# Performance work log

Measured on AMD Instinct MI355X. Metric: run time of the kernel, lower is better.

The kernel has to match this reference:

```python
import math
import jax, jax.numpy as jnp
import numpy as np

N, B, C, H, K = 1024, 8, 512, 8, 5  # seq len, batch, d_model, heads, near_kth
NEG = -1.0e9


def setup_inputs() -> dict:
    key = jax.random.key(0)
    ks = jax.random.split(key, 10)
    s = 0.02
    return {
        "query": jax.random.normal(ks[0], (N, B, C), jnp.float32),
        "key_t": jax.random.normal(ks[1], (N, B, C), jnp.float32),
        "value": jax.random.normal(ks[2], (N, B, C), jnp.float32),
        "src_position": jax.random.normal(ks[3], (N, B, 3), jnp.float32),
        "tgt_position": jax.random.normal(ks[4], (N, B, 3), jnp.float32),
        # nn.MultiheadAttention params (in_proj split into q/k/v, plus out_proj)
        "Wq": jax.random.normal(ks[5], (C, C), jnp.float32) * s,
        "Wk": jax.random.normal(ks[6], (C, C), jnp.float32) * s,
        "Wv": jax.random.normal(ks[7], (C, C), jnp.float32) * s,
        "bq": jnp.zeros((C,), jnp.float32),
        "bk": jnp.zeros((C,), jnp.float32),
        "bv": jnp.zeros((C,), jnp.float32),
        "Wo": jax.random.normal(ks[8], (C, C), jnp.float32) * s,
        "bo": jnp.zeros((C,), jnp.float32),
    }


def reference(query, key_t, value, src_position, tgt_position,
              Wq, Wk, Wv, bq, bk, bv, Wo, bo):
    # --- 'nearby' positional mask ---------------------------------------
    # dist[b, tgt, src] = ||src_position[src,b] - tgt_position[tgt,b]||^2
    diff = src_position[None, :, :, :] - tgt_position[:, None, :, :]  # (Nt,Ns,B,3)
    dist = jnp.sum(diff * diff, axis=-1).transpose(2, 0, 1)           # (B,Nt,Ns)
    # torch: topk(dist, k=5, dim=1, largest=False) -> 5 nearest TARGETS per source
    _, idx = jax.lax.top_k(-dist.transpose(0, 2, 1), K)               # (B,Ns,K) tgt idx
    mask = jnp.full((B, N, N), NEG, jnp.float32)
    b_i = jnp.arange(B)[:, None, None]
    s_i = jnp.arange(N)[None, :, None]
    mask = mask.at[b_i, idx, s_i].set(0.0)                            # (B,Nt,Ns)

    # --- multihead attention (eval mode, dropout=0) ----------------------
    hd = C // H
    scale = 1.0 / math.sqrt(hd)
    q = ((query @ Wq.T + bq) * scale).reshape(N, B, H, hd)
    k = (key_t @ Wk.T + bk).reshape(N, B, H, hd)
    v = (value @ Wv.T + bv).reshape(N, B, H, hd)
    scores = jnp.einsum('tbhd,sbhd->bhts', q, k) + mask[:, None]      # (B,H,Nt,Ns)
    attn = jax.nn.softmax(scores, axis=-1)
    ctx = jnp.einsum('bhts,sbhd->tbhd', attn, v).reshape(N, B, C)
    out = ctx @ Wo.T + bo                                             # (N,B,C)
    attn_avg = attn.mean(axis=1)                                      # (B,Nt,Ns)
    return out, attn_avg
```

## Files before the change

kernel.cpp:

```cpp
#include <hip/hip_runtime.h>
#include <cstdint>
#include <cstddef>

#define NSEQ 1024
#define BATCH 8
#define CMODEL 512
#define NHEAD 8
#define HDIM 64
#define CAP 64
#define FLTMAX 3.402823466e+38f

typedef short bf16x8 __attribute__((ext_vector_type(8)));
typedef float f32x4 __attribute__((ext_vector_type(4)));
typedef unsigned short ushort8v __attribute__((ext_vector_type(8)));
typedef unsigned short ushort2v __attribute__((ext_vector_type(2)));
typedef unsigned long long u64;

__device__ inline unsigned short f2bf(float f) {
    unsigned int u = __builtin_bit_cast(unsigned int, f);
    u += 0x7fffu + ((u >> 16) & 1u);
    return (unsigned short)(u >> 16);
}
__device__ inline float bf2f(unsigned short u) {
    return __builtin_bit_cast(float, (unsigned int)u << 16);
}

#define GLDS16(gsrc, ldst) \
    __builtin_amdgcn_global_load_lds((const __attribute__((address_space(1))) void*)(gsrc), \
                                     (__attribute__((address_space(3))) void*)(ldst), 16, 0, 0)

__global__ __launch_bounds__(256) void prepA(const float* __restrict__ w0,
                                             const float* __restrict__ w1,
                                             const float* __restrict__ w2,
                                             const float* __restrict__ w3,
                                             const float* __restrict__ value,
                                             const float* __restrict__ tgtp,
                                             const float* __restrict__ srcp,
                                             unsigned short* __restrict__ o0,
                                             unsigned short* __restrict__ o1,
                                             unsigned short* __restrict__ o2,
                                             unsigned short* __restrict__ o3,
                                             unsigned int* __restrict__ zp,
                                             float* __restrict__ vm_raw,
                                             float* __restrict__ tgt_soa,
                                             float* __restrict__ src_soa) {
    const int bid = blockIdx.x;
    const int tid = threadIdx.x;
    if (bid < 512) {
        const int idx = bid * 256 + tid;
        const int seg = idx >> 15;
        const int c   = idx & 32767;
        const float* src = seg == 0 ? w0 : seg == 1 ? w1 : seg == 2 ? w2 : w3;
        unsigned short* dst = seg == 0 ? o0 : seg == 1 ? o1 : seg == 2 ? o2 : o3;
        const float4 v0 = *(const float4*)(src + (size_t)c * 8);
        const float4 v1 = *(const float4*)(src + (size_t)c * 8 + 4);
        ushort8v u;
        u[0] = f2bf(v0.x); u[1] = f2bf(v0.y); u[2] = f2bf(v0.z); u[3] = f2bf(v0.w);
        u[4] = f2bf(v1.x); u[5] = f2bf(v1.y); u[6] = f2bf(v1.z); u[7] = f2bf(v1.w);
        *(ushort8v*)(dst + (size_t)c * 8) = u;
        return;
    }
    if (bid < 544) {
        zp[(bid - 512) * 256 + tid] = 0u;
        return;
    }
    if (bid < 608) {
        const int cb = bid - 544;
        const int b = cb >> 3, cg = cb & 7;
        const int ts = tid >> 6, c = cg * 64 + (tid & 63);
        float s = 0.f;
        for (int i = 0; i < 256; ++i) {
            const int t = ts * 256 + i;
            s += value[((size_t)t * BATCH + b) * CMODEL + c];
        }
        __shared__ float sh[4][64];
        sh[ts][tid & 63] = s;
        __syncthreads();
        if (ts == 0)
            vm_raw[b * CMODEL + c] = sh[0][tid & 63] + sh[1][tid & 63] +
                                     sh[2][tid & 63] + sh[3][tid & 63];
        return;
    }
    const int tb = bid - 608;
    const int which = tb >> 3, b = tb & 7;
    const float* src = which == 0 ? tgtp : srcp;
    float* dst = which == 0 ? tgt_soa : src_soa;
    for (int t = tid; t < NSEQ; t += 256) {
        const float* p = src + ((size_t)t * BATCH + b) * 3;
        dst[(b * 3 + 0) * NSEQ + t] = p[0];
        dst[(b * 3 + 1) * NSEQ + t] = p[1];
        dst[(b * 3 + 2) * NSEQ + t] = p[2];
    }
}

#define CX64(a, b) { const bool _c = (a) < (b); const u64 _mn = _c ? (a) : (b); \
                     const u64 _mx = _c ? (b) : (a); (a) = _mn; (b) = _mx; }

__global__ __launch_bounds__(256) void megaB(const float* __restrict__ a0,
                                             const float* __restrict__ a1,
                                             const float* __restrict__ a2,
                                             unsigned short* __restrict__ oa0,
                                             unsigned short* __restrict__ oa1,
                                             unsigned short* __restrict__ oa2,
                                             const float* __restrict__ src_soa,
                                             const float* __restrict__ tgt_soa,
                                             int* __restrict__ row_cnt,
                                             int* __restrict__ row_list,
                                             const unsigned short* __restrict__ Wv,
                                             const float* __restrict__ bv,
                                             const float* __restrict__ vm_raw,
                                             float* __restrict__ vm) {
    const int p = blockIdx.x;
    const int tid = threadIdx.x;

    if (p < 32) {
        const int bsel = p >> 2, quad = p & 3;
        const int w = tid >> 6, lane = tid & 63;
        const float* vr = vm_raw + bsel * CMODEL;
        const float4 va = *(const float4*)(vr + lane * 8);
        const float4 vb = *(const float4*)(vr + lane * 8 + 4);
        float vp[8] = {va.x, va.y, va.z, va.w, vb.x, vb.y, vb.z, vb.w};
        for (int i = 0; i < 32; ++i) {
            const int c = quad * 128 + w * 32 + i;
            const ushort8v wv = *(const ushort8v*)(Wv + (size_t)c * CMODEL + lane * 8);
            float s = 0.f;
            #pragma unroll
            for (int j = 0; j < 8; ++j) s += vp[j] * bf2f(wv[j]);
            #pragma unroll
            for (int off = 1; off < 64; off <<= 1) s += __shfl_xor(s, off);
            if (lane == 0) vm[bsel * CMODEL + c] = s * (1.f / (float)NSEQ) + bv[c];
        }
        return;
    }

    if (p >= 2080) {
        const unsigned int idx = (unsigned int)(p - 2080) * 256u + tid;
        const unsigned int seg = idx >> 19;
        const unsigned int c   = idx & 524287u;
        const float* src = seg == 0 ? a0 : seg == 1 ? a1 : a2;
        unsigned short* dst = seg == 0 ? oa0 : seg == 1 ? oa1 : oa2;
        const float4 v0 = *(const float4*)(src + (size_t)c * 8);
        const float4 v1 = *(const float4*)(src + (size_t)c * 8 + 4);
        ushort8v u;
        u[0] = f2bf(v0.x); u[1] = f2bf(v0.y); u[2] = f2bf(v0.z); u[3] = f2bf(v0.w);
        u[4] = f2bf(v1.x); u[5] = f2bf(v1.y); u[6] = f2bf(v1.z); u[7] = f2bf(v1.w);
        *(ushort8v*)(dst + (size_t)c * 8) = u;
        return;
    }

    const int w = tid >> 6, lane = tid & 63;
    const int wg = (p - 32) * 4 + w;
    const int s = wg & 1023, b = wg >> 10;

    const float* tx = tgt_soa + (b * 3 + 0) * NSEQ;
    const float* ty = tgt_soa + (b * 3 + 1) * NSEQ;
    const float* tz = tgt_soa + (b * 3 + 2) * NSEQ;
    const float sx = src_soa[(b * 3 + 0) * NSEQ + s];
    const float sy = src_soa[(b * 3 + 1) * NSEQ + s];
    const float sz = src_soa[(b * 3 + 2) * NSEQ + s];

    u64 v0 = ~0ull, v1 = ~0ull, v2 = ~0ull, v3 = ~0ull, v4 = ~0ull;

    #pragma unroll
    for (int i = 0; i < 16; ++i) {
        const int t = i * 64 + lane;
        const float dx = tx[t] - sx;
        const float dy = ty[t] - sy;
        const float dz = tz[t] - sz;
        const float d = dx * dx + dy * dy + dz * dz;
        u64 x = ((u64)__builtin_bit_cast(unsigned int, d) << 32) | (unsigned int)t;
        if (x < v4) {
            CX64(v0, x);
            CX64(v1, x);
            CX64(v2, x);
            CX64(v3, x);
            CX64(v4, x);
        }
    }

    #pragma unroll
    for (int off = 1; off < 64; off <<= 1) {
        const u64 p0 = __shfl_xor(v4, off);
        const u64 p1 = __shfl_xor(v3, off);
        const u64 p2 = __shfl_xor(v2, off);
        const u64 p3 = __shfl_xor(v1, off);
        const u64 p4 = __shfl_xor(v0, off);
        v0 = v0 < p0 ? v0 : p0;
        v1 = v1 < p1 ? v1 : p1;
        v2 = v2 < p2 ? v2 : p2;
        v3 = v3 < p3 ? v3 : p3;
        v4 = v4 < p4 ? v4 : p4;
        CX64(v0, v1); CX64(v3, v4); CX64(v2, v4); CX64(v2, v3); CX64(v1, v4);
        CX64(v0, v3); CX64(v0, v2); CX64(v1, v3); CX64(v1, v2);
    }

    if (lane == 0) {
        const u64 win[5] = {v0, v1, v2, v3, v4};
        #pragma unroll
        for (int k = 0; k < 5; ++k) {
            const int tt = (int)(unsigned int)win[k];
            const int pos = atomicAdd(&row_cnt[b * NSEQ + tt], 1);
            if (pos < CAP) row_list[((size_t)b * NSEQ + tt) * CAP + pos] = s;
        }
    }
}

__global__ __launch_bounds__(256, 3) void gemm_proj(const unsigned short* __restrict__ Aq,
                                                    const unsigned short* __restrict__ Ak,
                                                    const unsigned short* __restrict__ Av,
                                                    const unsigned short* __restrict__ Wq,
                                                    const unsigned short* __restrict__ Wk,
                                                    const unsigned short* __restrict__ Wv,
                                                    const float* __restrict__ bq,
                                                    const float* __restrict__ bk,
                                                    const float* __restrict__ bv,
                                                    unsigned short* __restrict__ oq,
                                                    unsigned short* __restrict__ ok,
                                                    unsigned short* __restrict__ ov) {
    __shared__ __align__(16) unsigned short smem[3 * 8192];
    const int p = blockIdx.x;
    const int logical = (p & 7) * 96 + (p >> 3);
    const int z = logical >> 8;
    const int r = logical & 255;
    const int m0 = (r >> 2) * 128, n0 = (r & 3) * 128;
    const unsigned short* Abf = z == 0 ? Aq : z == 1 ? Ak : Av;
    const unsigned short* Wbf = z == 0 ? Wq : z == 1 ? Wk : Wv;
    const float* bias = z == 0 ? bq : z == 1 ? bk : bv;
    unsigned short* outp = z == 0 ? oq : z == 1 ? ok : ov;
    const float scale = z == 0 ? 0.125f : 1.0f;

    const int tid = threadIdx.x;
    const int l = tid & 63, w = tid >> 6;
    const int wr = (w >> 1) * 64, wc = (w & 1) * 64;
    const int lr = l & 15, g = l >> 4;

    f32x4 acc[4][4] = {};

    const int rowX = tid >> 2;
    const int kg0  = (tid & 3) ^ ((rowX >> 1) & 3);
    const unsigned short* aS0 = Abf + (size_t)(m0 + rowX) * CMODEL + kg0 * 8;
    const unsigned short* aS1 = aS0 + (size_t)64 * CMODEL;
    const unsigned short* bS0 = Wbf + (size_t)(n0 + rowX) * CMODEL + kg0 * 8;
    const unsigned short* bS1 = bS0 + (size_t)64 * CMODEL;
    const int wb = w * 512;

    auto STAGE = [&](int k0, int buf) {
        unsigned short* bb = smem + buf * 8192;
        GLDS16(aS0 + k0, bb + wb);
        GLDS16(aS1 + k0, bb + 2048 + wb);
        GLDS16(bS0 + k0, bb + 4096 + wb);
        GLDS16(bS1 + k0, bb + 6144 + wb);
    };
    auto COMPUTE = [&](const unsigned short* base) {
        bf16x8 af[4], bg[4];
        #pragma unroll
        for (int i = 0; i < 4; ++i) {
            const int ra = wr + i * 16 + lr;
            af[i] = *(const bf16x8*)(base + ra * 32 + ((g ^ ((ra >> 1) & 3)) << 3));
        }
        #pragma unroll
        for (int j = 0; j < 4; ++j) {
            const int rb = wc + j * 16 + lr;
            bg[j] = *(const bf16x8*)(base + 4096 + rb * 32 + ((g ^ ((rb >> 1) & 3)) << 3));
        }
        #pragma unroll
        for (int i = 0; i < 4; ++i)
            #pragma unroll
            for (int j = 0; j < 4; ++j)
                acc[i][j] = __builtin_amdgcn_mfma_f32_16x16x32_bf16(af[i], bg[j], acc[i][j], 0, 0, 0);
    };

    STAGE(0, 0);
    STAGE(32, 1);

    int cur = 0;
    for (int t = 0; t < 15; ++t) {
        asm volatile("s_waitcnt vmcnt(4)" ::: "memory");
        __builtin_amdgcn_s_barrier();
        if (t < 14) {
            int nb = cur + 2; if (nb >= 3) nb -= 3;
            STAGE((t + 2) * 32, nb);
        }
        COMPUTE(smem + cur * 8192);
        ++cur; if (cur == 3) cur = 0;
    }
    asm volatile("s_waitcnt vmcnt(0)" ::: "memory");
    __builtin_amdgcn_s_barrier();
    COMPUTE(smem + cur * 8192);

    #pragma unroll
    for (int i = 0; i < 4; ++i) {
        #pragma unroll
        for (int j = 0; j < 4; ++j) {
            const int col = n0 + wc + j * 16 + lr;
            const float bcol = bias[col];
            #pragma unroll
            for (int rr = 0; rr < 4; ++rr) {
                const int row = m0 + wr + i * 16 + g * 4 + rr;
                const float val = (acc[i][j][rr] + bcol) * scale;
                const int t = row >> 3, bb = row & 7;
                outp[((size_t)(bb * NSEQ + t)) * CMODEL + col] = f2bf(val);
            }
        }
    }
}

__global__ __launch_bounds__(256, 3) void gemm_out(const unsigned short* __restrict__ Abf,
                                                   const unsigned short* __restrict__ Wbf,
                                                   const float* __restrict__ bias,
                                                   float* __restrict__ out) {
    __shared__ __align__(16) unsigned short smem[3 * 6144];
    const int p = blockIdx.x;
    const int logical = (p & 7) * 64 + (p >> 3);
    const int m0 = (logical >> 3) * 128, n0 = (logical & 7) * 64;

    const int tid = threadIdx.x;
    const int l = tid & 63, w = tid >> 6;
    const int wr = (w >> 1) * 64, wc = (w & 1) * 32;
    const int lr = l & 15, g = l >> 4;

    f32x4 acc[4][2] = {};

    const int rowX = tid >> 2;
    const int kg0  = (tid & 3) ^ ((rowX >> 1) & 3);
    const unsigned short* aS0 = Abf + (size_t)(m0 + rowX) * CMODEL + kg0 * 8;
    const unsigned short* aS1 = aS0 + (size_t)64 * CMODEL;
    const unsigned short* bS0 = Wbf + (size_t)(n0 + rowX) * CMODEL + kg0 * 8;
    const int wb = w * 512;

    auto STAGE = [&](int k0, int buf) {
        unsigned short* bb = smem + buf * 6144;
        GLDS16(aS0 + k0, bb + wb);
        GLDS16(aS1 + k0, bb + 2048 + wb);
        GLDS16(bS0 + k0, bb + 4096 + wb);
    };
    auto COMPUTE = [&](const unsigned short* base) {
        bf16x8 af[4], bg[2];
        #pragma unroll
        for (int i = 0; i < 4; ++i) {
            const int ra = wr + i * 16 + lr;
            af[i] = *(const bf16x8*)(base + ra * 32 + ((g ^ ((ra >> 1) & 3)) << 3));
        }
        #pragma unroll
        for (int j = 0; j < 2; ++j) {
            const int rb = wc + j * 16 + lr;
            bg[j] = *(const bf16x8*)(base + 4096 + rb * 32 + ((g ^ ((rb >> 1) & 3)) << 3));
        }
        #pragma unroll
        for (int i = 0; i < 4; ++i)
            #pragma unroll
            for (int j = 0; j < 2; ++j)
                acc[i][j] = __builtin_amdgcn_mfma_f32_16x16x32_bf16(af[i], bg[j], acc[i][j], 0, 0, 0);
    };

    STAGE(0, 0);
    STAGE(32, 1);

    int cur = 0;
    for (int t = 0; t < 15; ++t) {
        asm volatile("s_waitcnt vmcnt(3)" ::: "memory");
        __builtin_amdgcn_s_barrier();
        if (t < 14) {
            int nb = cur + 2; if (nb >= 3) nb -= 3;
            STAGE((t + 2) * 32, nb);
        }
        COMPUTE(smem + cur * 6144);
        ++cur; if (cur == 3) cur = 0;
    }
    asm volatile("s_waitcnt vmcnt(0)" ::: "memory");
    __builtin_amdgcn_s_barrier();
    COMPUTE(smem + cur * 6144);

    #pragma unroll
    for (int i = 0; i < 4; ++i) {
        #pragma unroll
        for (int j = 0; j < 2; ++j) {
            const int col = n0 + wc + j * 16 + lr;
            const float bcol = bias[col];
            #pragma unroll
            for (int r = 0; r < 4; ++r) {
                const int row = m0 + wr + i * 16 + g * 4 + r;
                out[(size_t)row * CMODEL + col] = acc[i][j][r] + bcol;
            }
        }
    }
}

__global__ __launch_bounds__(256) void sparse_attn(const unsigned short* __restrict__ q_ws,
                                                   const unsigned short* __restrict__ k_ws,
                                                   const unsigned short* __restrict__ v_ws,
                                                   const int* __restrict__ row_cnt,
                                                   const int* __restrict__ row_list,
                                                   const float* __restrict__ vm,
                                                   unsigned short* __restrict__ ctx,
                                                   float* __restrict__ attn_out) {
    const int t = blockIdx.x;
    const int b = blockIdx.y;
    const int tid = threadIdx.x;

    int cnt = row_cnt[b * NSEQ + t];
    if (cnt > CAP) cnt = CAP;

    float* arow = attn_out + ((size_t)b * NSEQ + t) * NSEQ;

    if (cnt == 0) {
        const float u = 1.f / (float)NSEQ;
        const float4 uv = {u, u, u, u};
        ((float4*)arow)[tid] = uv;
        for (int c = tid; c < CMODEL; c += 256)
            ctx[((size_t)t * BATCH + b) * CMODEL + c] = f2bf(vm[b * CMODEL + c]);
        return;
    }

    {
        const float4 zv = {0.f, 0.f, 0.f, 0.f};
        ((float4*)arow)[tid] = zv;
    }

    __shared__ float qs[CMODEL];
    __shared__ float esc[CAP][8];
    __shared__ float denom[8];
    __shared__ int   slist[CAP];

    if (tid < 8) denom[tid] = 0.f;
    if (tid < cnt) slist[tid] = row_list[((size_t)b * NSEQ + t) * CAP + tid];
    {
        const ushort2v qv = *(const ushort2v*)(q_ws + ((size_t)b * NSEQ + t) * CMODEL + tid * 2);
        qs[tid * 2] = bf2f(qv[0]); qs[tid * 2 + 1] = bf2f(qv[1]);
    }
    __syncthreads();

    const int wid = tid >> 6, lane = tid & 63;
    for (int i = wid; i < cnt; i += 4) {
        const int s = slist[i];
        const ushort8v kv = *(const ushort8v*)(k_ws + ((size_t)b * NSEQ + s) * CMODEL + lane * 8);
        const float* qrow = qs + lane * 8;
        float part = 0.f;
        #pragma unroll
        for (int j = 0; j < 8; ++j) part += qrow[j] * bf2f(kv[j]);
        part += __shfl_xor(part, 1);
        part += __shfl_xor(part, 2);
        part += __shfl_xor(part, 4);
        if ((lane & 7) == 0) {
            const int h = lane >> 3;
            const float e = __expf(part);
            esc[i][h] = e;
            atomicAdd(&denom[h], e);
        }
    }
    __syncthreads();

    for (int x = tid; x < cnt * 8; x += 256)
        esc[x >> 3][x & 7] /= denom[x & 7];
    __syncthreads();

    for (int i = tid; i < cnt; i += 256) {
        float pm = 0.f;
        #pragma unroll
        for (int h = 0; h < 8; ++h) pm += esc[i][h];
        arow[slist[i]] = pm * 0.125f;
    }

    const int c0 = tid * 2;
    const int h0 = c0 >> 6;
    float acc0 = 0.f, acc1 = 0.f;
    for (int i = 0; i < cnt; ++i) {
        const int s = slist[i];
        const float p = esc[i][h0];
        const ushort2v vv = *(const ushort2v*)(v_ws + ((size_t)b * NSEQ + s) * CMODEL + c0);
        acc0 += p * bf2f(vv[0]); acc1 += p * bf2f(vv[1]);
    }
    unsigned short* crow = ctx + ((size_t)t * BATCH + b) * CMODEL;
    ushort2v cv; cv[0] = f2bf(acc0); cv[1] = f2bf(acc1);
    *(ushort2v*)(crow + c0) = cv;
}

extern "C" void kernel_launch(void* const* d_in, const int* in_sizes, int n_in,
                              void* d_out, int out_size, void* d_ws, size_t ws_size,
                              hipStream_t stream) {
    (void)in_sizes; (void)n_in; (void)out_size; (void)ws_size;

    const float* query = (const float*)d_in[0];
    const float* key_t = (const float*)d_in[1];
    const float* value = (const float*)d_in[2];
    const float* srcp  = (const float*)d_in[3];
    const float* tgtp  = (const float*)d_in[4];
    const float* Wq    = (const float*)d_in[5];
    const float* Wk    = (const float*)d_in[6];
    const float* Wv    = (const float*)d_in[7];
    const float* bq    = (const float*)d_in[8];
    const float* bk    = (const float*)d_in[9];
    const float* bv    = (const float*)d_in[10];
    const float* Wo    = (const float*)d_in[11];
    const float* bo    = (const float*)d_in[12];

    float* out      = (float*)d_out;
    float* attn_out = out + (size_t)NSEQ * BATCH * CMODEL;

    const size_t NBC = (size_t)BATCH * NSEQ * CMODEL;
    const size_t WSZ = (size_t)CMODEL * CMODEL;
    unsigned short* q_ws  = (unsigned short*)d_ws;
    unsigned short* k_ws  = q_ws + NBC;
    unsigned short* v_ws  = k_ws + NBC;
    unsigned short* ctxbf = v_ws + NBC;
    unsigned short* qbf   = ctxbf + NBC;
    unsigned short* kbf   = qbf + NBC;
    unsigned short* vbf   = kbf + NBC;
    unsigned short* wqbf  = vbf + NBC;
    unsigned short* wkbf  = wqbf + WSZ;
    unsigned short* wvbf  = wkbf + WSZ;
    unsigned short* wobf  = wvbf + WSZ;
    int*   row_cnt  = (int*)(wobf + WSZ);
    float* vm       = (float*)(row_cnt + BATCH * NSEQ);
    float* vm_raw   = vm + BATCH * CMODEL;
    float* tgt_soa  = vm_raw + BATCH * CMODEL;
    float* src_soa  = tgt_soa + (size_t)BATCH * 3 * NSEQ;
    int*   row_list = (int*)(src_soa + (size_t)BATCH * 3 * NSEQ);

    prepA<<<624, 256, 0, stream>>>(Wq, Wk, Wv, Wo, value, tgtp, srcp,
                                   wqbf, wkbf, wvbf, wobf,
                                   (unsigned int*)row_cnt, vm_raw,
                                   tgt_soa, src_soa);

    megaB<<<8224, 256, 0, stream>>>(query, key_t, value, qbf, kbf, vbf,
                                    src_soa, tgt_soa, row_cnt, row_list,
                                    wvbf, bv, vm_raw, vm);

    gemm_proj<<<768, 256, 0, stream>>>(qbf, kbf, vbf,
                                       wqbf, wkbf, wvbf,
                                       bq, bk, bv,
                                       q_ws, k_ws, v_ws);

    sparse_attn<<<dim3(NSEQ, BATCH), 256, 0, stream>>>(q_ws, k_ws, v_ws, row_cnt,
                                                       row_list, vm, ctxbf, attn_out);

    gemm_out<<<512, 256, 0, stream>>>(ctxbf, wobf, bo, out);
}
```

Baseline: 94.37 us.

## Rebalance prep work across kernels and interleave topk with activation casts

The weight bf16 casts and the value column-sum move out of the small prepA launch into megaB, so prepA only zeroes counters and transposes positions. The vm projection moves from megaB into extra blocks of the projection GEMM kernel, after vm_raw is ready. Inside megaB, blocks alternate one top-k block with three activation-cast blocks, mixing compute-light atomic work with bandwidth-bound streaming. This aims to shorten the serial prep kernel and improve overlap, at the cost of more branch-heavy block dispatch and GEMM-kernel blocks doing unrelated work.

Result: slower. 136.7 us (+44.9%).

```diff
diff --git a/kernel.cpp b/kernel.cpp
--- a/kernel.cpp
+++ b/kernel.cpp
@@ -29,59 +29,18 @@
     __builtin_amdgcn_global_load_lds((const __attribute__((address_space(1))) void*)(gsrc), \
                                      (__attribute__((address_space(3))) void*)(ldst), 16, 0, 0)
 
-__global__ __launch_bounds__(256) void prepA(const float* __restrict__ w0,
-                                             const float* __restrict__ w1,
-                                             const float* __restrict__ w2,
-                                             const float* __restrict__ w3,
-                                             const float* __restrict__ value,
-                                             const float* __restrict__ tgtp,
+__global__ __launch_bounds__(256) void prepA(const float* __restrict__ tgtp,
                                              const float* __restrict__ srcp,
-                                             unsigned short* __restrict__ o0,
-                                             unsigned short* __restrict__ o1,
-                                             unsigned short* __restrict__ o2,
-                                             unsigned short* __restrict__ o3,
                                              unsigned int* __restrict__ zp,
-                                             float* __restrict__ vm_raw,
                                              float* __restrict__ tgt_soa,
                                              float* __restrict__ src_soa) {
     const int bid = blockIdx.x;
     const int tid = threadIdx.x;
-    if (bid < 512) {
-        const int idx = bid * 256 + tid;
-        const int seg = idx >> 15;
-        const int c   = idx & 32767;
-        const float* src = seg == 0 ? w0 : seg == 1 ? w1 : seg == 2 ? w2 : w3;
-        unsigned short* dst = seg == 0 ? o0 : seg == 1 ? o1 : seg == 2 ? o2 : o3;
-        const float4 v0 = *(const float4*)(src + (size_t)c * 8);
-        const float4 v1 = *(const float4*)(src + (size_t)c * 8 + 4);
-        ushort8v u;
-        u[0] = f2bf(v0.x); u[1] = f2bf(v0.y); u[2] = f2bf(v0.z); u[3] = f2bf(v0.w);
-        u[4] = f2bf(v1.x); u[5] = f2bf(v1.y); u[6] = f2bf(v1.z); u[7] = f2bf(v1.w);
-        *(ushort8v*)(dst + (size_t)c * 8) = u;
+    if (bid < 32) {
+        zp[bid * 256 + tid] = 0u;
         return;
     }
-    if (bid < 544) {
-        zp[(bid - 512) * 256 + tid] = 0u;
-        return;
-    }
-    if (bid < 608) {
-        const int cb = bid - 544;
-        const int b = cb >> 3, cg = cb & 7;
-        const int ts = tid >> 6, c = cg * 64 + (tid & 63);
-        float s = 0.f;
-        for (int i = 0; i < 256; ++i) {
-            const int t = ts * 256 + i;
-            s += value[((size_t)t * BATCH + b) * CMODEL + c];
-        }
-        __shared__ float sh[4][64];
-        sh[ts][tid & 63] = s;
-        __syncthreads();
-        if (ts == 0)
-            vm_raw[b * CMODEL + c] = sh[0][tid & 63] + sh[1][tid & 63] +
-                                     sh[2][tid & 63] + sh[3][tid & 63];
-        return;
-    }
-    const int tb = bid - 608;
+    const int tb = bid - 32;
     const int which = tb >> 3, b = tb & 7;
     const float* src = which == 0 ? tgtp : srcp;
     float* dst = which == 0 ? tgt_soa : src_soa;
@@ -102,19 +61,149 @@
                                              unsigned short* __restrict__ oa0,
                                              unsigned short* __restrict__ oa1,
                                              unsigned short* __restrict__ oa2,
+                                             const float* __restrict__ w0,
+                                             const float* __restrict__ w1,
+                                             const float* __restrict__ w2,
+                                             const float* __restrict__ w3,
+                                             unsigned short* __restrict__ o0,
+                                             unsigned short* __restrict__ o1,
+                                             unsigned short* __restrict__ o2,
+                                             unsigned short* __restrict__ o3,
+                                             const float* __restrict__ value,
+                                             float* __restrict__ vm_raw,
                                              const float* __restrict__ src_soa,
                                              const float* __restrict__ tgt_soa,
                                              int* __restrict__ row_cnt,
-                                             int* __restrict__ row_list,
-                                             const unsigned short* __restrict__ Wv,
-                                             const float* __restrict__ bv,
-                                             const float* __restrict__ vm_raw,
-                                             float* __restrict__ vm) {
+                                             int* __restrict__ row_list) {
     const int p = blockIdx.x;
     const int tid = threadIdx.x;
 
-    if (p < 32) {
-        const int bsel = p >> 2, quad = p & 3;
+    if (p >= 8192) {
+        if (p < 8704) {
+            const int idx = (p - 8192) * 256 + tid;
+            const int seg = idx >> 15;
+            const int c   = idx & 32767;
+            const float* src = seg == 0 ? w0 : seg == 1 ? w1 : seg == 2 ? w2 : w3;
+            unsigned short* dst = seg == 0 ? o0 : seg == 1 ? o1 : seg == 2 ? o2 : o3;
+            const float4 v0 = *(const float4*)(src + (size_t)c * 8);
+            const float4 v1 = *(const float4*)(src + (size_t)c * 8 + 4);
+            ushort8v u;
+            u[0] = f2bf(v0.x); u[1] = f2bf(v0.y); u[2] = f2bf(v0.z); u[3] = f2bf(v0.w);
+            u[4] = f2bf(v1.x); u[5] = f2bf(v1.y); u[6] = f2bf(v1.z); u[7] = f2bf(v1.w);
+            *(ushort8v*)(dst + (size_t)c * 8) = u;
+        } else {
+            const int cb = p - 8704;
+            const int b = cb >> 3, cg = cb & 7;
+            const int ts = tid >> 6, c = cg * 64 + (tid & 63);
+            float s = 0.f;
+            for (int i = 0; i < 256; ++i) {
+                const int t = ts * 256 + i;
+                s += value[((size_t)t * BATCH + b) * CMODEL + c];
+            }
+            __shared__ float sh[4][64];
+            sh[ts][tid & 63] = s;
+            __syncthreads();
+            if (ts == 0)
+                vm_raw[b * CMODEL + c] = sh[0][tid & 63] + sh[1][tid & 63] +
+                                         sh[2][tid & 63] + sh[3][tid & 63];
+        }
+        return;
+    }
+
+    const int q = p >> 2, r = p & 3;
+
+    if (r != 0) {
+        const unsigned int idx = (unsigned int)(3 * q + r - 1) * 256u + tid;
+        const unsigned int seg = idx >> 19;
+        const unsigned int c   = idx & 524287u;
+        const float* src = seg == 0 ? a0 : seg == 1 ? a1 : a2;
+        unsigned short* dst = seg == 0 ? oa0 : seg == 1 ? oa1 : oa2;
+        const float4 v0 = *(const float4*)(src + (size_t)c * 8);
+        const float4 v1 = *(const float4*)(src + (size_t)c * 8 + 4);
+        ushort8v u;
+        u[0] = f2bf(v0.x); u[1] = f2bf(v0.y); u[2] = f2bf(v0.z); u[3] = f2bf(v0.w);
+        u[4] = f2bf(v1.x); u[5] = f2bf(v1.y); u[6] = f2bf(v1.z); u[7] = f2bf(v1.w);
+        *(ushort8v*)(dst + (size_t)c * 8) = u;
+        return;
+    }
+
+    const int w = tid >> 6, lane = tid & 63;
+    const int wg = q * 4 + w;
+    const int s = wg & 1023, b = wg >> 10;
+
+    const float* tx = tgt_soa + (b * 3 + 0) * NSEQ;
+    const float* ty = tgt_soa + (b * 3 + 1) * NSEQ;
+    const float* tz = tgt_soa + (b * 3 + 2) * NSEQ;
+    const float sx = src_soa[(b * 3 + 0) * NSEQ + s];
+    const float sy = src_soa[(b * 3 + 1) * NSEQ + s];
+    const float sz = src_soa[(b * 3 + 2) * NSEQ + s];
+
+    u64 v0 = ~0ull, v1 = ~0ull, v2 = ~0ull, v3 = ~0ull, v4 = ~0ull;
+
+    #pragma unroll
+    for (int i = 0; i < 16; ++i) {
+        const int t = i * 64 + lane;
+        const float dx = tx[t] - sx;
+        const float dy = ty[t] - sy;
+        const float dz = tz[t] - sz;
+        const float d = dx * dx + dy * dy + dz * dz;
+        u64 x = ((u64)__builtin_bit_cast(unsigned int, d) << 32) | (unsigned int)t;
+        if (x < v4) {
+            CX64(v0, x);
+            CX64(v1, x);
+            CX64(v2, x);
+            CX64(v3, x);
+            CX64(v4, x);
+        }
+    }
+
+    #pragma unroll
+    for (int off = 1; off < 64; off <<= 1) {
+        const u64 p0 = __shfl_xor(v4, off);
+        const u64 p1 = __shfl_xor(v3, off);
+        const u64 p2 = __shfl_xor(v2, off);
+        const u64 p3 = __shfl_xor(v1, off);
+        const u64 p4 = __shfl_xor(v0, off);
+        v0 = v0 < p0 ? v0 : p0;
+        v1 = v1 < p1 ? v1 : p1;
+        v2 = v2 < p2 ? v2 : p2;
+        v3 = v3 < p3 ? v3 : p3;
+        v4 = v4 < p4 ? v4 : p4;
+        CX64(v0, v1); CX64(v3, v4); CX64(v2, v4); CX64(v2, v3); CX64(v1, v4);
+        CX64(v0, v3); CX64(v0, v2); CX64(v1, v3); CX64(v1, v2);
+    }
+
+    if (lane == 0) {
+        const u64 win[5] = {v0, v1, v2, v3, v4};
+        #pragma unroll
+        for (int k = 0; k < 5; ++k) {
+            const int tt = (int)(unsigned int)win[k];
+            const int pos = atomicAdd(&row_cnt[b * NSEQ + tt], 1);
+            if (pos < CAP) row_list[((size_t)b * NSEQ + tt) * CAP + pos] = s;
+        }
+    }
+}
+
+__global__ __launch_bounds__(256, 3) void gemm_projG(const unsigned short* __restrict__ Aq,
+                                                     const unsigned short* __restrict__ Ak,
+                                                     const unsigned short* __restrict__ Av,
+                                                     const unsigned short* __restrict__ Wq,
+                                                     const unsigned short* __restrict__ Wk,
+                                                     const unsigned short* __restrict__ Wv,
+                                                     const float* __restrict__ bq,
+                                                     const float* __restrict__ bk,
+                                                     const float* __restrict__ bv,
+                                                     unsigned short* __restrict__ oq,
+                                                     unsigned short* __restrict__ ok,
+                                                     unsigned short* __restrict__ ov,
+                                                     const float* __restrict__ vm_raw,
+                                                     float* __restrict__ vm) {
+    const int p = blockIdx.x;
+    const int tid = threadIdx.x;
+
+    if (p >= 768) {
+        const int pb = p - 768;
+        const int bsel = pb >> 2, quad = pb & 3;
         const int w = tid >> 6, lane = tid & 63;
         const float* vr = vm_raw + bsel * CMODEL;
         const float4 va = *(const float4*)(vr + lane * 8);
@@ -133,92 +222,7 @@
         return;
     }
 
-    if (p >= 2080) {
-        const unsigned int idx = (unsigned int)(p - 2080) * 256u + tid;
-        const unsigned int seg = idx >> 19;
-        const unsigned int c   = idx & 524287u;
-        const float* src = seg == 0 ? a0 : seg == 1 ? a1 : a2;
-        unsigned short* dst = seg == 0 ? oa0 : seg == 1 ? oa1 : oa2;
-        const float4 v0 = *(const float4*)(src + (size_t)c * 8);
-        const float4 v1 = *(const float4*)(src + (size_t)c * 8 + 4);
-        ushort8v u;
-        u[0] = f2bf(v0.x); u[1] = f2bf(v0.y); u[2] = f2bf(v0.z); u[3] = f2bf(v0.w);
-        u[4] = f2bf(v1.x); u[5] = f2bf(v1.y); u[6] = f2bf(v1.z); u[7] = f2bf(v1.w);
-        *(ushort8v*)(dst + (size_t)c * 8) = u;
-        return;
-    }
-
-    const int w = tid >> 6, lane = tid & 63;
-    const int wg = (p - 32) * 4 + w;
-    const int s = wg & 1023, b = wg >> 10;
-
-    const float* tx = tgt_soa + (b * 3 + 0) * NSEQ;
-    const float* ty = tgt_soa + (b * 3 + 1) * NSEQ;
-    const float* tz = tgt_soa + (b * 3 + 2) * NSEQ;
-    const float sx = src_soa[(b * 3 + 0) * NSEQ + s];
-    const float sy = src_soa[(b * 3 + 1) * NSEQ + s];
-    const float sz = src_soa[(b * 3 + 2) * NSEQ + s];
-
-    u64 v0 = ~0ull, v1 = ~0ull, v2 = ~0ull, v3 = ~0ull, v4 = ~0ull;
-
-    #pragma unroll
-    for (int i = 0; i < 16; ++i) {
-        const int t = i * 64 + lane;
-        const float dx = tx[t] - sx;
-        const float dy = ty[t] - sy;
-        const float dz = tz[t] - sz;
-        const float d = dx * dx + dy * dy + dz * dz;
-        u64 x = ((u64)__builtin_bit_cast(unsigned int, d) << 32) | (unsigned int)t;
-        if (x < v4) {
-            CX64(v0, x);
-            CX64(v1, x);
-            CX64(v2, x);
-            CX64(v3, x);
-            CX64(v4, x);
-        }
-    }
-
-    #pragma unroll
-    for (int off = 1; off < 64; off <<= 1) {
-        const u64 p0 = __shfl_xor(v4, off);
-        const u64 p1 = __shfl_xor(v3, off);
-        const u64 p2 = __shfl_xor(v2, off);
-        const u64 p3 = __shfl_xor(v1, off);
-        const u64 p4 = __shfl_xor(v0, off);
-        v0 = v0 < p0 ? v0 : p0;
-        v1 = v1 < p1 ? v1 : p1;
-        v2 = v2 < p2 ? v2 : p2;
-        v3 = v3 < p3 ? v3 : p3;
-        v4 = v4 < p4 ? v4 : p4;
-        CX64(v0, v1); CX64(v3, v4); CX64(v2, v4); CX64(v2, v3); CX64(v1, v4);
-        CX64(v0, v3); CX64(v0, v2); CX64(v1, v3); CX64(v1, v2);
-    }
-
-    if (lane == 0) {
-        const u64 win[5] = {v0, v1, v2, v3, v4};
-        #pragma unroll
-        for (int k = 0; k < 5; ++k) {
-            const int tt = (int)(unsigned int)win[k];
-            const int pos = atomicAdd(&row_cnt[b * NSEQ + tt], 1);
-            if (pos < CAP) row_list[((size_t)b * NSEQ + tt) * CAP + pos] = s;
-        }
-    }
-}
-
-__global__ __launch_bounds__(256, 3) void gemm_proj(const unsigned short* __restrict__ Aq,
-                                                    const unsigned short* __restrict__ Ak,
-                                                    const unsigned short* __restrict__ Av,
-                                                    const unsigned short* __restrict__ Wq,
-                                                    const unsigned short* __restrict__ Wk,
-                                                    const unsigned short* __restrict__ Wv,
-                                                    const float* __restrict__ bq,
-                                                    const float* __restrict__ bk,
-                                                    const float* __restrict__ bv,
-                                                    unsigned short* __restrict__ oq,
-                                                    unsigned short* __restrict__ ok,
-                                                    unsigned short* __restrict__ ov) {
     __shared__ __align__(16) unsigned short smem[3 * 8192];
-    const int p = blockIdx.x;
     const int logical = (p & 7) * 96 + (p >> 3);
     const int z = logical >> 8;
     const int r = logical & 255;
@@ -229,7 +233,6 @@
     unsigned short* outp = z == 0 ? oq : z == 1 ? ok : ov;
     const float scale = z == 0 ? 0.125f : 1.0f;
 
-    const int tid = threadIdx.x;
     const int l = tid & 63, w = tid >> 6;
     const int wr = (w >> 1) * 64, wc = (w & 1) * 64;
     const int lr = l & 15, g = l >> 4;
@@ -517,19 +520,19 @@
     float* src_soa  = tgt_soa + (size_t)BATCH * 3 * NSEQ;
     int*   row_list = (int*)(src_soa + (size_t)BATCH * 3 * NSEQ);
 
-    prepA<<<624, 256, 0, stream>>>(Wq, Wk, Wv, Wo, value, tgtp, srcp,
-                                   wqbf, wkbf, wvbf, wobf,
-                                   (unsigned int*)row_cnt, vm_raw,
-                                   tgt_soa, src_soa);
-
-    megaB<<<8224, 256, 0, stream>>>(query, key_t, value, qbf, kbf, vbf,
-                                    src_soa, tgt_soa, row_cnt, row_list,
-                                    wvbf, bv, vm_raw, vm);
-
-    gemm_proj<<<768, 256, 0, stream>>>(qbf, kbf, vbf,
-                                       wqbf, wkbf, wvbf,
-                                       bq, bk, bv,
-                                       q_ws, k_ws, v_ws);
+    prepA<<<48, 256, 0, stream>>>(tgtp, srcp, (unsigned int*)row_cnt,
+                                  tgt_soa, src_soa);
+
+    megaB<<<8768, 256, 0, stream>>>(query, key_t, value, qbf, kbf, vbf,
+                                    Wq, Wk, Wv, Wo, wqbf, wkbf, wvbf, wobf,
+                                    value, vm_raw,
+                                    src_soa, tgt_soa, row_cnt, row_list);
+
+    gemm_projG<<<800, 256, 0, stream>>>(qbf, kbf, vbf,
+                                        wqbf, wkbf, wvbf,
+                                        bq, bk, bv,
+                                        q_ws, k_ws, v_ws,
+                                        vm_raw, vm);
 
     sparse_attn<<<dim3(NSEQ, BATCH), 256, 0, stream>>>(q_ws, k_ws, v_ws, row_cnt,
                                                        row_list, vm, ctxbf, attn_out);
```
